# Performance work log

Hardware: AMD Instinct MI355X
Metric: run time of the kernel (lower is better)

Reference implementation:

```python
import jax, jax.numpy as jnp
import numpy as np

NUM_HEADS = 12
DIM = 768


def setup_inputs() -> dict:
    key = jax.random.key(0)
    ks = jax.random.split(key, 7)
    B, S, E = 8, 1024, DIM
    s = 0.02
    return {
        "x": jax.random.normal(ks[0], (B, S, E), dtype=jnp.float32),
        "Wq": jax.random.normal(ks[1], (E, E), dtype=jnp.float32) * s,
        "bq": jnp.zeros((E,), dtype=jnp.float32),
        "Wk": jax.random.normal(ks[2], (E, E), dtype=jnp.float32) * s,
        "bk": jnp.zeros((E,), dtype=jnp.float32),
        "Wo": jax.random.normal(ks[3], (E, E), dtype=jnp.float32) * s,
        "bo": jnp.zeros((E,), dtype=jnp.float32),
    }


def reference(x, Wq, bq, Wk, bk, Wo, bo):
    B, S, E = x.shape
    n = NUM_HEADS
    d = E // n
    scale = d ** (-0.5)

    def heads(t):  # [B,S,E] -> [B,n,S,d]
        return t.reshape(B, S, n, d).transpose(0, 2, 1, 3)

    q = heads(x @ Wq.T + bq)
    k = heads(x @ Wk.T + bk)
    v = k  # faithful to source bug: v = self.k_w(x)

    attn = jnp.einsum('bnqd,bnkd->bnqk', q, k) * scale  # [B,n,S,S]
    attn = jax.nn.softmax(attn, axis=-1)
    out = jnp.einsum('bnqk,bnkd->bnqd', attn, v)  # [B,n,S,d]
    out = out.transpose(0, 2, 1, 3).reshape(B, S, E)
    return out @ Wo.T + bo
```

## Files before the change

kernel.cpp:

```cpp
#include <hip/hip_runtime.h>
#include <stdint.h>


using short8   = __attribute__((ext_vector_type(8))) short;
using uint4v   = __attribute__((ext_vector_type(4))) unsigned;
using float4v  = __attribute__((ext_vector_type(4))) float;
using float16v = __attribute__((ext_vector_type(16))) float;

struct __align__(8) U2 { unsigned x, y; };

__device__ __forceinline__ void async16(void* lds, const void* g) {
  __builtin_amdgcn_global_load_lds(
      (const __attribute__((address_space(1))) void*)g,
      (__attribute__((address_space(3))) void*)lds, 16, 0, 0);
}

#define LGKM_WAIT  asm volatile("s_waitcnt lgkmcnt(0)" ::: "memory")
#define BARRIER    asm volatile("s_barrier" ::: "memory")

template <int N> __device__ __forceinline__ void vm_wait() {
  if constexpr (N == 4) asm volatile("s_waitcnt vmcnt(4)" ::: "memory");
  else if constexpr (N == 0) asm volatile("s_waitcnt vmcnt(0)" ::: "memory");
}

__device__ __forceinline__ unsigned bf16b(float f) {
  union { float f; unsigned u; } v; v.f = f;
  unsigned r = v.u + 0x7FFFu + ((v.u >> 16) & 1u);
  return r >> 16;
}
__device__ __forceinline__ unsigned rne_adj(float f) {
  union { float f; unsigned u; } v; v.f = f;
  return v.u + 0x7FFFu + ((v.u >> 16) & 1u);
}
__device__ __forceinline__ unsigned pack_hi16(unsigned a, unsigned b) {
  return __builtin_amdgcn_perm(a, b, 0x07060302u);
}
__device__ __forceinline__ unsigned cvt_pk_bf16(float a, float b) {
  unsigned r;
  asm("v_cvt_pk_bf16_f32 %0, %1, %2" : "=v"(r) : "v"(a), "v"(b));
  return r;
}

__global__ __launch_bounds__(256) void cvt_all(
    const float* __restrict__ x, const float* __restrict__ w0,
    const float* __restrict__ w1, const float* __restrict__ w2,
    unsigned short* __restrict__ ox, unsigned short* __restrict__ o0,
    unsigned short* __restrict__ o1, unsigned short* __restrict__ o2) {
  const int bid = blockIdx.x;
  const float* in;
  unsigned short* out;
  int i;
  if (bid < 3072) {
    in = x; out = ox; i = bid * 256 + threadIdx.x;
  } else {
    int b2 = bid - 3072;
    int mi = b2 / 288;
    in = (mi == 0) ? w0 : (mi == 1) ? w1 : w2;
    out = (mi == 0) ? o0 : (mi == 1) ? o1 : o2;
    i = (b2 - mi * 288) * 256 + threadIdx.x;
  }
  const float4v* p = (const float4v*)in;
  float4v a = p[i * 2], b = p[i * 2 + 1];
  uint4v w;
  w[0] = pack_hi16(rne_adj(a[1]), rne_adj(a[0]));
  w[1] = pack_hi16(rne_adj(a[3]), rne_adj(a[2]));
  w[2] = pack_hi16(rne_adj(b[1]), rne_adj(b[0]));
  w[3] = pack_hi16(rne_adj(b[3]), rne_adj(b[2]));
  ((uint4v*)out)[i] = w;
}

template <int BUF, int WAIT, class F1, class F2, class F3, class F4>
__device__ __forceinline__ void ktile4(const char* lds, int aoff, int boff,
                                       float4v (&acc)[2][2][2][4],
                                       F1&& s1, F2&& s2, F3&& s3, F4&& s4) {
  constexpr int AB = BUF * 65536;
  constexpr int BB = BUF * 65536 + 32768;
  short8 af[2][2], b0[4][2], b1[4][2];

#define RD_A(MH)                                                              \
  _Pragma("unroll") for (int mf = 0; mf < 2; ++mf)                            \
  _Pragma("unroll") for (int ks = 0; ks < 2; ++ks)                            \
    af[mf][ks] = *(const short8*)(lds + AB + (MH)*16384 + aoff + mf*2048 + ks*64);
#define RD_B(NH, BF)                                                          \
  _Pragma("unroll") for (int nf = 0; nf < 4; ++nf)                            \
  _Pragma("unroll") for (int ks = 0; ks < 2; ++ks)                            \
    BF[nf][ks] = *(const short8*)(lds + BB + (NH)*16384 + boff + nf*2048 + ks*64);
#define MM(MH, NH, BF)                                                        \
  _Pragma("unroll") for (int mf = 0; mf < 2; ++mf)                            \
  _Pragma("unroll") for (int nf = 0; nf < 4; ++nf)                            \
  _Pragma("unroll") for (int ks = 0; ks < 2; ++ks)                            \
    acc[MH][NH][mf][nf] = __builtin_amdgcn_mfma_f32_16x16x32_bf16(            \
        af[mf][ks], BF[nf][ks], acc[MH][NH][mf][nf], 0, 0, 0);

  RD_A(0) RD_B(0, b0) s1();
  BARRIER; LGKM_WAIT; __builtin_amdgcn_sched_barrier(0);
  __builtin_amdgcn_s_setprio(1); MM(0, 0, b0) __builtin_amdgcn_s_setprio(0);
  BARRIER;
  RD_B(1, b1) s2();
  BARRIER; LGKM_WAIT; __builtin_amdgcn_sched_barrier(0);
  __builtin_amdgcn_s_setprio(1); MM(0, 1, b1) __builtin_amdgcn_s_setprio(0);
  BARRIER;
  RD_A(1) s3();
  BARRIER; LGKM_WAIT; __builtin_amdgcn_sched_barrier(0);
  __builtin_amdgcn_s_setprio(1); MM(1, 1, b1) __builtin_amdgcn_s_setprio(0);
  BARRIER;
  s4();
  BARRIER; LGKM_WAIT; __builtin_amdgcn_sched_barrier(0);
  __builtin_amdgcn_s_setprio(1); MM(1, 0, b0) __builtin_amdgcn_s_setprio(0);
  vm_wait<WAIT>();
  BARRIER;
#undef RD_A
#undef RD_B
#undef MM
}

__global__ __launch_bounds__(512, 2) void sgemm_qk8(
    const unsigned short* __restrict__ A, const unsigned short* __restrict__ B,
    const float* __restrict__ bias0, const float* __restrict__ bias1,
    unsigned short* __restrict__ outq, unsigned short* __restrict__ outk,
    unsigned short* __restrict__ outkt) {
  extern __shared__ __align__(16) char lds[];
  const int tid = threadIdx.x;
  const int w = tid >> 6, lane = tid & 63;
  const int Q4 = lane >> 4, r = lane & 15;
  const int wr = w & 3, wc = w >> 2;
  const int bid = blockIdx.x;
  const int wg = (bid & 7) * 24 + (bid >> 3);
  const int m0 = (wg / 6) * 256;
  const int n0 = (wg % 6) * 256;

  const int srow = lane >> 3;
  const int scol = ((lane & 7) * 8) ^ ((lane >> 5) * 16);

  auto stA = [&](int buf, int half, int t) {
#pragma unroll
    for (int j = 0; j < 2; ++j)
      async16(lds + buf * 65536 + half * 16384 + (w * 2 + j) * 1024 + lane * 16,
              A + (size_t)(m0 + half * 128 + (w * 2 + j) * 8 + srow) * 768 +
                  t * 64 + scol);
  };
  auto stB = [&](int buf, int half, int t) {
#pragma unroll
    for (int j = 0; j < 2; ++j)
      async16(lds + buf * 65536 + 32768 + half * 16384 + (w * 2 + j) * 1024 + lane * 16,
              B + (size_t)(n0 + half * 128 + (w * 2 + j) * 8 + srow) * 768 +
                  t * 64 + scol);
  };

  const int flip = ((lane >> 2) & 1) * 32;
  const int aoff = (wr * 32 + r) * 128 + ((Q4 * 16) ^ flip);
  const int boff = (wc * 64 + r) * 128 + ((Q4 * 16) ^ flip);

  float4v acc[2][2][2][4];
#pragma unroll
  for (int a = 0; a < 2; ++a)
#pragma unroll
    for (int b = 0; b < 2; ++b)
#pragma unroll
      for (int c = 0; c < 2; ++c)
#pragma unroll
        for (int d = 0; d < 4; ++d)
#pragma unroll
          for (int g = 0; g < 4; ++g) acc[a][b][c][d][g] = 0.0f;

  stA(0, 0, 0); stB(0, 0, 0); stB(0, 1, 0); stA(0, 1, 0);
  stA(1, 0, 1); stB(1, 1, 1);
  vm_wait<4>(); BARRIER;

#pragma unroll 1
  for (int i = 0; i < 5; ++i) {
    const int t1 = 2 * i + 1, t2 = 2 * i + 2, t3 = 2 * i + 3;
    ktile4<0, 4>(lds, aoff, boff, acc,
                 [&] { stA(1, 1, t1); stB(1, 0, t1); },
                 [&] {},
                 [&] { stA(0, 0, t2); },
                 [&] { stB(0, 1, t2); });
    ktile4<1, 4>(lds, aoff, boff, acc,
                 [&] { stA(0, 1, t2); stB(0, 0, t2); },
                 [&] {},
                 [&] { stA(1, 0, t3); },
                 [&] { stB(1, 1, t3); });
  }
  ktile4<0, 0>(lds, aoff, boff, acc,
               [&] { stA(1, 1, 11); stB(1, 0, 11); },
               [&] {}, [&] {}, [&] {});
  ktile4<1, -1>(lds, aoff, boff, acc, [&] {}, [&] {}, [&] {}, [&] {});

  const bool isq = (n0 < 768);
  const float* bias = isq ? bias0 : bias1;
  unsigned short* outp = isq ? outq : outk;
  const int nb = isq ? n0 : (n0 - 768);
  const float scl = isq ? 0.18033688011112042f : 1.0f;
#pragma unroll
  for (int Nh = 0; Nh < 2; ++Nh)
#pragma unroll
    for (int nf = 0; nf < 4; ++nf) {
      const int n = nb + Nh * 128 + wc * 64 + nf * 16 + r;
      const float bv = bias[n];
#pragma unroll
      for (int Mh = 0; Mh < 2; ++Mh)
#pragma unroll
        for (int mf = 0; mf < 2; ++mf) {
          const int m = m0 + Mh * 128 + wr * 32 + mf * 16 + Q4 * 4;
#pragma unroll
          for (int g = 0; g < 4; ++g)
            outp[(size_t)(m + g) * 768 + n] =
                (unsigned short)bf16b((acc[Mh][Nh][mf][nf][g] + bv) * scl);
        }
    }
  if (!isq) {
    const int bq = m0 >> 10;
    const int sb0 = (m0 & 1023) + wr * 32 + (Q4 & 1) * 8 + (Q4 >> 1) * 4;
#pragma unroll
    for (int Nh = 0; Nh < 2; ++Nh)
#pragma unroll
      for (int nf = 0; nf < 4; ++nf) {
        const int nk = nb + Nh * 128 + wc * 64 + nf * 16 + r;
        const int hh = nk >> 6, dd = nk & 63;
        const float bv = bias1[nk];
#pragma unroll
        for (int Mh = 0; Mh < 2; ++Mh)
#pragma unroll
          for (int mf = 0; mf < 2; ++mf) {
            const int ns = sb0 + Mh * 128 + mf * 16;
            const float4v a4 = acc[Mh][Nh][mf][nf];
            unsigned lo = pack_hi16(rne_adj(a4[1] + bv), rne_adj(a4[0] + bv));
            unsigned hi = pack_hi16(rne_adj(a4[3] + bv), rne_adj(a4[2] + bv));
            *(U2*)(outkt + (size_t)((bq * 12 + hh) * 64 + dd) * 1024 + ns) =
                U2{lo, hi};
          }
      }
  }
}

__global__ __launch_bounds__(512, 6) void sgemm_out(
    const unsigned short* __restrict__ A, const unsigned short* __restrict__ B,
    const float* __restrict__ bias, float* __restrict__ outp) {
  __shared__ __align__(16) unsigned short a_l[4096];
  __shared__ __align__(16) unsigned short b_l[8192];
  const int tid = threadIdx.x;
  const int w = tid >> 6, lane = tid & 63;
  const int Q4 = lane >> 4, r = lane & 15;
  const int m0 = blockIdx.y * 64;
  const int n0 = blockIdx.x * 128;
  const int wm = w >> 2, wn = w & 3;

  float4v acc[2][2];
#pragma unroll
  for (int i = 0; i < 2; ++i)
#pragma unroll
    for (int j = 0; j < 2; ++j)
#pragma unroll
      for (int g = 0; g < 4; ++g) acc[i][j][g] = 0.0f;

  const unsigned short* Ab = A + (size_t)(m0 + r) * 768 + Q4 * 8;
  const unsigned short* Bb = B + (size_t)(n0 + r) * 768 + Q4 * 8;

  uint4v ra, rb[2];
  auto gload = [&](int kt) {
    ra = *(const uint4v*)(Ab + (w >> 1) * 12288 + kt + (w & 1) * 32);
#pragma unroll
    for (int ci = 0; ci < 2; ++ci) {
      int idx = w * 2 + ci;
      rb[ci] = *(const uint4v*)(Bb + (idx >> 1) * 12288 + kt + (idx & 1) * 32);
    }
  };
  auto swrite = [&]() {
    *(uint4v*)&a_l[w * 512 + lane * 8] = ra;
#pragma unroll
    for (int ci = 0; ci < 2; ++ci) {
      int idx = w * 2 + ci;
      *(uint4v*)&b_l[idx * 512 + lane * 8] = rb[ci];
    }
  };

  short8 af[2][2], bf[2][2];
  auto loadf = [&]() {
#pragma unroll
    for (int i = 0; i < 2; ++i)
#pragma unroll
      for (int ks = 0; ks < 2; ++ks)
        af[i][ks] = *(const short8*)&a_l[((wm * 2 + i) * 2 + ks) * 512 + lane * 8];
#pragma unroll
    for (int j = 0; j < 2; ++j)
#pragma unroll
      for (int ks = 0; ks < 2; ++ks)
        bf[j][ks] = *(const short8*)&b_l[((wn * 2 + j) * 2 + ks) * 512 + lane * 8];
  };
  auto dot = [&]() {
#pragma unroll
    for (int mt = 0; mt < 2; ++mt)
#pragma unroll
      for (int nt = 0; nt < 2; ++nt)
#pragma unroll
        for (int ks = 0; ks < 2; ++ks)
          acc[mt][nt] = __builtin_amdgcn_mfma_f32_16x16x32_bf16(
              af[mt][ks], bf[nt][ks], acc[mt][nt], 0, 0, 0);
  };

  gload(0);
#pragma unroll 1
  for (int t = 0; t < 12; ++t) {
    if (t > 0) BARRIER;
    swrite();
    if (t < 11) gload(t * 64 + 64);
    LGKM_WAIT;
    BARRIER;
    loadf();
    dot();
  }

#pragma unroll
  for (int nt = 0; nt < 2; ++nt) {
    int n = n0 + wn * 32 + nt * 16 + r;
    float bv = bias[n];
#pragma unroll
    for (int mt = 0; mt < 2; ++mt) {
      int m = m0 + wm * 32 + mt * 16 + Q4 * 4;
#pragma unroll
      for (int g = 0; g < 4; ++g)
        outp[(size_t)(m + g) * 768 + n] = acc[mt][nt][g] + bv;
    }
  }
}

__global__ __launch_bounds__(256, 3) void attn_fused(
    const unsigned short* __restrict__ qg,
    const unsigned short* __restrict__ kg,
    const unsigned short* __restrict__ ktg,
    unsigned short* __restrict__ ao) {
  __shared__ __align__(16) unsigned short q_l[8192];
  __shared__ __align__(16) unsigned short k_l[8192];
  __shared__ __align__(16) unsigned short vt_l[8192];

  const int tid = threadIdx.x;
  const int w = tid >> 6, lane = tid & 63;
  const int l31 = lane & 31, hi = lane >> 5;
  const int bid = blockIdx.x;
  const int b = bid & 7;
  const int h = bid >> 6;
  const int qt = (bid >> 3) & 7;
  const int q0 = qt * 128;
  const int bh = b * 12 + h;

#pragma unroll
  for (int ci = 0; ci < 4; ++ci) {
    int c = w * 4 + ci;
    async16(&q_l[c * 512 + lane * 8],
            qg + ((size_t)(b * 1024 + q0 + (c >> 2) * 32 + l31) * 768 + h * 64 + (c & 3) * 16 + hi * 8));
    async16(&k_l[c * 512 + lane * 8],
            kg + ((size_t)(b * 1024 + (c >> 2) * 32 + l31) * 768 + h * 64 + (c & 3) * 16 + hi * 8));
    async16(&vt_l[c * 512 + lane * 8],
            ktg + ((size_t)(bh * 64 + (c >> 3) * 32 + l31) * 1024 + (c & 7) * 16 + hi * 8));
  }
  __syncthreads();

  short8 bfq[4];
#pragma unroll
  for (int kb = 0; kb < 4; ++kb)
    bfq[kb] = *(const short8*)&q_l[(w * 4 + kb) * 512 + lane * 8];

  float16v o_acc[2];
#pragma unroll
  for (int db = 0; db < 2; ++db)
#pragma unroll
    for (int e = 0; e < 16; ++e) o_acc[db][e] = 0.0f;
  float ps0 = 0.0f, ps1 = 0.0f, ps2 = 0.0f, ps3 = 0.0f;

#pragma unroll 1
  for (int it = 0; it < 8; ++it) {
    float16v sc[4];
#pragma unroll
    for (int sb = 0; sb < 4; ++sb)
#pragma unroll
      for (int e = 0; e < 16; ++e) sc[sb][e] = 0.0f;
    __builtin_amdgcn_s_setprio(1);
#pragma unroll
    for (int sb = 0; sb < 4; ++sb)
#pragma unroll
      for (int kb = 0; kb < 4; ++kb) {
        short8 af = *(const short8*)&k_l[(sb * 4 + kb) * 512 + lane * 8];
        sc[sb] = __builtin_amdgcn_mfma_f32_32x32x16_bf16(af, bfq[kb], sc[sb], 0, 0, 0);
      }
    __builtin_amdgcn_s_setprio(0);

    short8 pf0[4], pf1[4];
#pragma unroll
    for (int sb = 0; sb < 4; ++sb) {
      float pe[16];
#pragma unroll
      for (int e = 0; e < 16; ++e) pe[e] = __builtin_amdgcn_exp2f(sc[sb][e]);
#pragma unroll
      for (int e = 0; e < 16; e += 4) {
        ps0 += pe[e]; ps1 += pe[e + 1]; ps2 += pe[e + 2]; ps3 += pe[e + 3];
      }
      uint4v w0, w1;
#pragma unroll
      for (int p = 0; p < 4; ++p) {
        w0[p] = cvt_pk_bf16(pe[2 * p], pe[2 * p + 1]);
        w1[p] = cvt_pk_bf16(pe[2 * p + 8], pe[2 * p + 9]);
      }
      pf0[sb] = __builtin_bit_cast(short8, w0);
      pf1[sb] = __builtin_bit_cast(short8, w1);
    }

    BARRIER;
    if (it < 7) {
      const int s1 = (it + 1) * 128;
#pragma unroll
      for (int ci = 0; ci < 4; ++ci) {
        int c = w * 4 + ci;
        async16(&k_l[c * 512 + lane * 8],
                kg + ((size_t)(b * 1024 + s1 + (c >> 2) * 32 + l31) * 768 + h * 64 + (c & 3) * 16 + hi * 8));
      }
      vm_wait<4>();
    } else {
      vm_wait<0>();
    }
    BARRIER;

    __builtin_amdgcn_s_setprio(1);
#pragma unroll
    for (int sb = 0; sb < 4; ++sb)
#pragma unroll
      for (int db = 0; db < 2; ++db) {
        short8 vf0 = *(const short8*)&vt_l[(db * 8 + sb * 2) * 512 + lane * 8];
        o_acc[db] = __builtin_amdgcn_mfma_f32_32x32x16_bf16(vf0, pf0[sb], o_acc[db], 0, 0, 0);
        short8 vf1 = *(const short8*)&vt_l[(db * 8 + sb * 2 + 1) * 512 + lane * 8];
        o_acc[db] = __builtin_amdgcn_mfma_f32_32x32x16_bf16(vf1, pf1[sb], o_acc[db], 0, 0, 0);
      }
    __builtin_amdgcn_s_setprio(0);

    if (it < 7) {
      BARRIER;
      const int s1 = (it + 1) * 128;
#pragma unroll
      for (int ci = 0; ci < 4; ++ci) {
        int c = w * 4 + ci;
        async16(&vt_l[c * 512 + lane * 8],
                ktg + ((size_t)(bh * 64 + (c >> 3) * 32 + l31) * 1024 + s1 + (c & 7) * 16 + hi * 8));
      }
      vm_wait<4>();
      BARRIER;
    }
  }

  float ps = (ps0 + ps1) + (ps2 + ps3);
  ps += __shfl_xor(ps, 32, 64);
  const float inv = 1.0f / ps;
  const size_t rowbase = (size_t)(b * 1024 + q0 + w * 32 + l31) * 768 + h * 64;
#pragma unroll
  for (int db = 0; db < 2; ++db)
#pragma unroll
    for (int qq = 0; qq < 4; ++qq) {
      unsigned lo = cvt_pk_bf16(o_acc[db][qq * 4 + 0] * inv,
                                o_acc[db][qq * 4 + 1] * inv);
      unsigned hh = cvt_pk_bf16(o_acc[db][qq * 4 + 2] * inv,
                                o_acc[db][qq * 4 + 3] * inv);
      *(U2*)(ao + rowbase + db * 32 + qq * 8 + hi * 4) = U2{lo, hh};
    }
}

extern "C" void kernel_launch(void* const* d_in, const int* in_sizes, int n_in,
                              void* d_out, int out_size, void* d_ws, size_t ws_size,
                              hipStream_t stream) {
  const float* x  = (const float*)d_in[0];
  const float* Wq = (const float*)d_in[1];
  const float* bq = (const float*)d_in[2];
  const float* Wk = (const float*)d_in[3];
  const float* bk = (const float*)d_in[4];
  const float* Wo = (const float*)d_in[5];
  const float* bo = (const float*)d_in[6];
  (void)in_sizes; (void)n_in; (void)out_size; (void)ws_size;

  static bool inited = false;
  if (!inited) {
    (void)hipFuncSetAttribute((const void*)sgemm_qk8,
                              hipFuncAttributeMaxDynamicSharedMemorySize, 131072);
    inited = true;
  }

  char* ws = (char*)d_ws;
  unsigned short* x_b   = (unsigned short*)(ws);
  unsigned short* wqk_b = (unsigned short*)(ws + 12582912);
  unsigned short* wo_b  = (unsigned short*)(ws + 14942208);
  unsigned short* q_b   = (unsigned short*)(ws + 16121856);
  unsigned short* k_b   = (unsigned short*)(ws + 28704768);
  unsigned short* kt_b  = (unsigned short*)(ws + 41287680);
  unsigned short* ao_b  = (unsigned short*)(ws + 53870592);

  cvt_all<<<3936, 256, 0, stream>>>(x, Wq, Wk, Wo,
                                    x_b, wqk_b, wqk_b + 589824, wo_b);

  sgemm_qk8<<<192, 512, 131072, stream>>>(x_b, wqk_b, bq, bk, q_b, k_b, kt_b);
  attn_fused<<<768, 256, 0, stream>>>(q_b, k_b, kt_b, ao_b);
  sgemm_out<<<dim3(6, 128), 512, 0, stream>>>(ao_b, wo_b, bo, (float*)d_out);
}
```

Measured before the change: 190.6 us.

## Double-buffer K tiles by reusing Q LDS buffer after Q registers load

Once Q fragments sit in registers, the Q shared-memory buffer is reused as a second K buffer, so the attention loop alternates between two K buffers. The K tile for step it+2 is prefetched together with the V tile for it+1, which removes the K load and its barrier wait from the middle of each iteration. The loop is unrolled by two so each half uses a fixed buffer. This adds more outstanding loads and relies on careful vmcnt accounting to stay correct.

```diff
diff --git a/kernel.cpp b/kernel.cpp
--- a/kernel.cpp
+++ b/kernel.cpp
@@ -19,7 +19,8 @@
 #define BARRIER    asm volatile("s_barrier" ::: "memory")
 
 template <int N> __device__ __forceinline__ void vm_wait() {
-  if constexpr (N == 4) asm volatile("s_waitcnt vmcnt(4)" ::: "memory");
+  if constexpr (N == 8) asm volatile("s_waitcnt vmcnt(8)" ::: "memory");
+  else if constexpr (N == 4) asm volatile("s_waitcnt vmcnt(4)" ::: "memory");
   else if constexpr (N == 0) asm volatile("s_waitcnt vmcnt(0)" ::: "memory");
 }
 
@@ -329,8 +330,8 @@
     const unsigned short* __restrict__ kg,
     const unsigned short* __restrict__ ktg,
     unsigned short* __restrict__ ao) {
+  __shared__ __align__(16) unsigned short k_l[8192];
   __shared__ __align__(16) unsigned short q_l[8192];
-  __shared__ __align__(16) unsigned short k_l[8192];
   __shared__ __align__(16) unsigned short vt_l[8192];
 
   const int tid = threadIdx.x;
@@ -343,22 +344,39 @@
   const int q0 = qt * 128;
   const int bh = b * 12 + h;
 
+  auto stageK = [&](unsigned short* dst, int s0) {
+#pragma unroll
+    for (int ci = 0; ci < 4; ++ci) {
+      int c = w * 4 + ci;
+      async16(&dst[c * 512 + lane * 8],
+              kg + ((size_t)(b * 1024 + s0 + (c >> 2) * 32 + l31) * 768 + h * 64 + (c & 3) * 16 + hi * 8));
+    }
+  };
+  auto stageV = [&](int s0) {
+#pragma unroll
+    for (int ci = 0; ci < 4; ++ci) {
+      int c = w * 4 + ci;
+      async16(&vt_l[c * 512 + lane * 8],
+              ktg + ((size_t)(bh * 64 + (c >> 3) * 32 + l31) * 1024 + s0 + (c & 7) * 16 + hi * 8));
+    }
+  };
+
 #pragma unroll
   for (int ci = 0; ci < 4; ++ci) {
     int c = w * 4 + ci;
     async16(&q_l[c * 512 + lane * 8],
             qg + ((size_t)(b * 1024 + q0 + (c >> 2) * 32 + l31) * 768 + h * 64 + (c & 3) * 16 + hi * 8));
-    async16(&k_l[c * 512 + lane * 8],
-            kg + ((size_t)(b * 1024 + (c >> 2) * 32 + l31) * 768 + h * 64 + (c & 3) * 16 + hi * 8));
-    async16(&vt_l[c * 512 + lane * 8],
-            ktg + ((size_t)(bh * 64 + (c >> 3) * 32 + l31) * 1024 + (c & 7) * 16 + hi * 8));
-  }
+  }
+  stageK(k_l, 0);
+  stageV(0);
   __syncthreads();
 
   short8 bfq[4];
 #pragma unroll
   for (int kb = 0; kb < 4; ++kb)
     bfq[kb] = *(const short8*)&q_l[(w * 4 + kb) * 512 + lane * 8];
+  LGKM_WAIT;
+  stageK(q_l, 128);
 
   float16v o_acc[2];
 #pragma unroll
@@ -367,8 +385,7 @@
     for (int e = 0; e < 16; ++e) o_acc[db][e] = 0.0f;
   float ps0 = 0.0f, ps1 = 0.0f, ps2 = 0.0f, ps3 = 0.0f;
 
-#pragma unroll 1
-  for (int it = 0; it < 8; ++it) {
+  auto one_iter = [&](int it, unsigned short* krd) {
     float16v sc[4];
 #pragma unroll
     for (int sb = 0; sb < 4; ++sb)
@@ -379,7 +396,7 @@
     for (int sb = 0; sb < 4; ++sb)
 #pragma unroll
       for (int kb = 0; kb < 4; ++kb) {
-        short8 af = *(const short8*)&k_l[(sb * 4 + kb) * 512 + lane * 8];
+        short8 af = *(const short8*)&krd[(sb * 4 + kb) * 512 + lane * 8];
         sc[sb] = __builtin_amdgcn_mfma_f32_32x32x16_bf16(af, bfq[kb], sc[sb], 0, 0, 0);
       }
     __builtin_amdgcn_s_setprio(0);
@@ -404,19 +421,7 @@
       pf1[sb] = __builtin_bit_cast(short8, w1);
     }
 
-    BARRIER;
-    if (it < 7) {
-      const int s1 = (it + 1) * 128;
-#pragma unroll
-      for (int ci = 0; ci < 4; ++ci) {
-        int c = w * 4 + ci;
-        async16(&k_l[c * 512 + lane * 8],
-                kg + ((size_t)(b * 1024 + s1 + (c >> 2) * 32 + l31) * 768 + h * 64 + (c & 3) * 16 + hi * 8));
-      }
-      vm_wait<4>();
-    } else {
-      vm_wait<0>();
-    }
+    if (it < 7) vm_wait<4>(); else vm_wait<0>();
     BARRIER;
 
     __builtin_amdgcn_s_setprio(1);
@@ -433,16 +438,21 @@
 
     if (it < 7) {
       BARRIER;
-      const int s1 = (it + 1) * 128;
-#pragma unroll
-      for (int ci = 0; ci < 4; ++ci) {
-        int c = w * 4 + ci;
-        async16(&vt_l[c * 512 + lane * 8],
-                ktg + ((size_t)(bh * 64 + (c >> 3) * 32 + l31) * 1024 + s1 + (c & 7) * 16 + hi * 8));
+      stageV((it + 1) * 128);
+      if (it < 6) {
+        stageK(krd, (it + 2) * 128);
+        vm_wait<8>();
+      } else {
+        vm_wait<4>();
       }
-      vm_wait<4>();
       BARRIER;
     }
+  };
+
+#pragma unroll 1
+  for (int tt = 0; tt < 4; ++tt) {
+    one_iter(2 * tt, k_l);
+    one_iter(2 * tt + 1, q_l);
   }
 
   float ps = (ps0 + ps1) + (ps2 + ps3);
```

New measurement: 271.8 us. 1.43x slower.
